# Kernel optimization log

Measured on AMD Instinct MI355X. Metric: run time of the kernel, lower is better.

The kernel has to match this reference:

```python
import jax, jax.numpy as jnp
import numpy as np

B, N, C = 2, 1024, 768
H = 12            # num_heads
HP = 24           # H_prime
HD = C // H       # head_dim = 64
KS = 3            # local conv kernel size
SCALE = HD ** -0.5


def setup_inputs() -> dict:
    key = jax.random.key(0)
    ks = jax.random.split(key, 9)
    s = lambda fan_in: 1.0 / np.sqrt(fan_in)
    return {
        "x": jax.random.normal(ks[0], (B, N, C), jnp.float32),
        "W_qk": jax.random.normal(ks[1], (2 * C, C), jnp.float32) * s(C),
        "W_v": jax.random.normal(ks[2], (C, C), jnp.float32) * s(C),
        "W_exp": jax.random.normal(ks[3], (HP, H), jnp.float32) * s(H),      # 1x1 conv H->HP
        "W_loc": jax.random.normal(ks[4], (HP, 1, KS, KS), jnp.float32) * s(KS * KS),  # depthwise 3x3
        "b_loc": jnp.zeros((HP,), jnp.float32),
        "W_red": jax.random.normal(ks[5], (H, HP), jnp.float32) * s(HP),    # 1x1 conv HP->H
        "W_proj": jax.random.normal(ks[6], (C, C), jnp.float32) * s(C),
        "b_proj": jnp.zeros((C,), jnp.float32),
    }


def _forward(x, W_qk, W_v, W_exp, W_loc, b_loc, W_red, W_proj, b_proj):
    b, n, c = x.shape
    # Attention: qk projection -> (2,B,H,N,HD)
    qk = (x @ W_qk.T).reshape(b, n, 2, H, HD).transpose(2, 0, 3, 1, 4)
    q, k = qk[0], qk[1]                                   # (B,H,N,HD)
    v = (x @ W_v.T).reshape(b, n, H, HD).transpose(0, 2, 1, 3)  # (B,H,N,HD)
    attn = jax.nn.softmax(jnp.einsum('bhnd,bhmd->bhnm', q, k) * SCALE, axis=-1)  # (B,H,N,N)

    # TokenSelector: conv-based reweighting of the attention map
    A_exp = jnp.einsum('oi,binm->bonm', W_exp, attn)      # 1x1 expand -> (B,HP,N,N)
    A_loc = jax.lax.conv_general_dilated(
        A_exp, W_loc, window_strides=(1, 1), padding='SAME',
        dimension_numbers=('NCHW', 'OIHW', 'NCHW'),
        feature_group_count=HP) + b_loc[None, :, None, None]
    A_loc = jax.nn.relu(A_loc)
    A_red = jnp.einsum('oi,binm->bonm', W_red, A_loc) * SCALE  # (B,H,N,N)
    attn2 = jax.nn.softmax(A_red, axis=-1)

    out = jnp.einsum('bhnm,bhmd->bhnd', attn2, v)         # (B,H,N,HD)
    out = out.transpose(0, 2, 1, 3).reshape(b, n, c)      # (B,N,C)
    out = out @ W_proj.T + b_proj
    return out, A_exp


def reference(x, W_qk, W_v, W_exp, W_loc, b_loc, W_red, W_proj, b_proj):
    return _forward(x, W_qk, W_v, W_exp, W_loc, b_loc, W_red, W_proj, b_proj)
```

## Files before the change

kernel.cpp:

```cpp
#include <hip/hip_runtime.h>
#include <math.h>

#define BB    2
#define NN    1024
#define CC    768
#define HH    12
#define HPP   24
#define HD    64
#define SCALE 0.125f

typedef float fvec4 __attribute__((ext_vector_type(4)));

#define SEG   (2*1024*768)
#define QOFF  0
#define KOFF  (SEG)
#define VOFF  (2*SEG)
#define HOFF  (3*SEG)

#define ASTR 132
#define BSTR 68

__global__ __launch_bounds__(256)
void qkv_gemm(const float* __restrict__ x, const float* __restrict__ Wqk,
              const float* __restrict__ Wv, float* __restrict__ ws)
{
    __shared__ float As[2][16*ASTR];
    __shared__ float Bs[2][16*BSTR];
    float* qtok = ws + QOFF;
    float* kt   = ws + KOFF;
    float* vws  = ws + VOFF;

    const int tid = threadIdx.x;
    const int bn  = blockIdx.x;
    const int bm  = blockIdx.y;
    const int tx  = tid & 15, ty = tid >> 4;

    const int am  = tid >> 1, ak = (tid & 1) * 8;
    const int bnr = tid >> 2, bk = (tid & 3) * 4;

    const float* Ap = x + (size_t)(bm*128 + am) * 768 + ak;
    const int jrow  = bn*64 + bnr;
    const float* Bp = (jrow < 1536) ? (Wqk + (size_t)jrow * 768 + bk)
                                    : (Wv  + (size_t)(jrow - 1536) * 768 + bk);

    float acc[8][4] = {};

    float4 a0 = *(const float4*)(Ap);
    float4 a1 = *(const float4*)(Ap + 4);
    float4 bv = *(const float4*)(Bp);
#pragma unroll
    for (int j = 0; j < 4; ++j) {
        As[0][(ak+j)*ASTR + am]   = ((const float*)&a0)[j];
        As[0][(ak+4+j)*ASTR + am] = ((const float*)&a1)[j];
        Bs[0][(bk+j)*BSTR + bnr]  = ((const float*)&bv)[j];
    }
    __syncthreads();

    for (int t = 0; t < 48; ++t) {
        const int cur = t & 1;
        if (t < 47) {
            a0 = *(const float4*)(Ap + (t+1)*16);
            a1 = *(const float4*)(Ap + (t+1)*16 + 4);
            bv = *(const float4*)(Bp + (t+1)*16);
        }
        const float* Asb = As[cur];
        const float* Bsb = Bs[cur];
#pragma unroll
        for (int kk = 0; kk < 16; ++kk) {
            float a[8], b[4];
#pragma unroll
            for (int i = 0; i < 8; ++i) a[i] = Asb[kk*ASTR + ty*8 + i];
#pragma unroll
            for (int j = 0; j < 4; ++j) b[j] = Bsb[kk*BSTR + tx*4 + j];
#pragma unroll
            for (int i = 0; i < 8; ++i)
#pragma unroll
                for (int j = 0; j < 4; ++j)
                    acc[i][j] = fmaf(a[i], b[j], acc[i][j]);
        }
        if (t < 47) {
#pragma unroll
            for (int j = 0; j < 4; ++j) {
                As[cur^1][(ak+j)*ASTR + am]   = ((const float*)&a0)[j];
                As[cur^1][(ak+4+j)*ASTR + am] = ((const float*)&a1)[j];
                Bs[cur^1][(bk+j)*BSTR + bnr]  = ((const float*)&bv)[j];
            }
        }
        __syncthreads();
    }

    const int colbase = bn*64 + tx*4;
    if (colbase < 768) {
#pragma unroll
        for (int i = 0; i < 8; ++i) {
            const int trow = bm*128 + ty*8 + i;
            float4 o = {acc[i][0], acc[i][1], acc[i][2], acc[i][3]};
            *(float4*)(qtok + (size_t)trow*768 + colbase) = o;
        }
    } else if (colbase < 1536) {
        const int p = colbase - 768;
#pragma unroll
        for (int i = 0; i < 8; ++i) {
            const int trow = bm*128 + ty*8 + i;
            const int b = trow >> 10, n = trow & 1023;
#pragma unroll
            for (int j = 0; j < 4; ++j)
                kt[((size_t)(b*768 + p + j))*NN + n] = acc[i][j];
        }
    } else {
        const int p = colbase - 1536;
#pragma unroll
        for (int i = 0; i < 8; ++i) {
            const int trow = bm*128 + ty*8 + i;
            const int b = trow >> 10, n = trow & 1023;
            float4 o = {acc[i][0], acc[i][1], acc[i][2], acc[i][3]};
            *(float4*)(vws + (((size_t)b*HH + (p >> 6))*NN + n)*HD + (p & 63)) = o;
        }
    }
}

__global__ __launch_bounds__(256, 2)
void attn_expand(const float* __restrict__ qtok, const float* __restrict__ kt,
                 const float* __restrict__ Wexp, float* __restrict__ aexp)
{
    __shared__ __align__(16) float qs[2*CC];
    __shared__ float wexp_s[HPP * HH];
    __shared__ float smax[2][HH * 4];
    __shared__ float ssum[2][HH * 4];

    const int tid  = threadIdx.x;
    const int lane = tid & 63, wid = tid >> 6;
    const int x    = blockIdx.x & 7;
    const int b    = x >> 2;
    const int np   = ((x & 3) << 7) | (blockIdx.x >> 3);
    const int n0   = np << 1;
    const int m4   = tid;

    const fvec4* qsrc = (const fvec4*)(qtok + (size_t)(b*NN + n0) * CC);
    ((fvec4*)qs)[tid] = qsrc[tid];
    if (tid < 128) ((fvec4*)qs)[256 + tid] = qsrc[256 + tid];
    for (int i2 = tid; i2 < HPP*HH; i2 += 256) wexp_s[i2] = Wexp[i2];
    __syncthreads();

    fvec4 l0[HH], l1[HH];
#pragma unroll
    for (int h = 0; h < HH; ++h) {
        fvec4 a0 = {0.f,0.f,0.f,0.f}, a1 = {0.f,0.f,0.f,0.f};
        const fvec4* kr = ((const fvec4*)kt) + (size_t)(b*768 + h*64) * 256 + m4;
        const float* q0p = qs + h*64;
        const float* q1p = qs + CC + h*64;
#pragma unroll 8
        for (int d = 0; d < 64; ++d) {
            const fvec4 kv = kr[(size_t)d * 256];
            const float qa = q0p[d];
            const float qb = q1p[d];
            a0.x = fmaf(kv.x, qa, a0.x); a0.y = fmaf(kv.y, qa, a0.y);
            a0.z = fmaf(kv.z, qa, a0.z); a0.w = fmaf(kv.w, qa, a0.w);
            a1.x = fmaf(kv.x, qb, a1.x); a1.y = fmaf(kv.y, qb, a1.y);
            a1.z = fmaf(kv.z, qb, a1.z); a1.w = fmaf(kv.w, qb, a1.w);
        }
        l0[h].x = a0.x*SCALE; l0[h].y = a0.y*SCALE;
        l0[h].z = a0.z*SCALE; l0[h].w = a0.w*SCALE;
        l1[h].x = a1.x*SCALE; l1[h].y = a1.y*SCALE;
        l1[h].z = a1.z*SCALE; l1[h].w = a1.w*SCALE;
    }

#pragma unroll
    for (int h = 0; h < HH; ++h) {
        float t0 = fmaxf(fmaxf(l0[h].x, l0[h].y), fmaxf(l0[h].z, l0[h].w));
        float t1 = fmaxf(fmaxf(l1[h].x, l1[h].y), fmaxf(l1[h].z, l1[h].w));
#pragma unroll
        for (int off = 32; off > 0; off >>= 1) {
            t0 = fmaxf(t0, __shfl_xor(t0, off, 64));
            t1 = fmaxf(t1, __shfl_xor(t1, off, 64));
        }
        if (lane == 0) { smax[0][h*4 + wid] = t0; smax[1][h*4 + wid] = t1; }
    }
    __syncthreads();

#pragma unroll
    for (int h = 0; h < HH; ++h) {
        const float m0 = fmaxf(fmaxf(smax[0][h*4+0], smax[0][h*4+1]),
                               fmaxf(smax[0][h*4+2], smax[0][h*4+3]));
        const float m1 = fmaxf(fmaxf(smax[1][h*4+0], smax[1][h*4+1]),
                               fmaxf(smax[1][h*4+2], smax[1][h*4+3]));
        l0[h].x = __expf(l0[h].x - m0); l0[h].y = __expf(l0[h].y - m0);
        l0[h].z = __expf(l0[h].z - m0); l0[h].w = __expf(l0[h].w - m0);
        l1[h].x = __expf(l1[h].x - m1); l1[h].y = __expf(l1[h].y - m1);
        l1[h].z = __expf(l1[h].z - m1); l1[h].w = __expf(l1[h].w - m1);
        float s0 = (l0[h].x + l0[h].y) + (l0[h].z + l0[h].w);
        float s1 = (l1[h].x + l1[h].y) + (l1[h].z + l1[h].w);
#pragma unroll
        for (int off = 32; off > 0; off >>= 1) {
            s0 += __shfl_xor(s0, off, 64);
            s1 += __shfl_xor(s1, off, 64);
        }
        if (lane == 0) { ssum[0][h*4 + wid] = s0; ssum[1][h*4 + wid] = s1; }
    }
    __syncthreads();

#pragma unroll
    for (int h = 0; h < HH; ++h) {
        const float i0 = 1.f / (ssum[0][h*4+0] + ssum[0][h*4+1] +
                                ssum[0][h*4+2] + ssum[0][h*4+3]);
        const float i1 = 1.f / (ssum[1][h*4+0] + ssum[1][h*4+1] +
                                ssum[1][h*4+2] + ssum[1][h*4+3]);
        l0[h].x *= i0; l0[h].y *= i0; l0[h].z *= i0; l0[h].w *= i0;
        l1[h].x *= i1; l1[h].y *= i1; l1[h].z *= i1; l1[h].w *= i1;
    }

    fvec4* ab = ((fvec4*)aexp) + ((size_t)b*HPP*NN + n0) * 256;
#pragma unroll 4
    for (int o = 0; o < HPP; ++o) {
        fvec4 e0 = {0.f,0.f,0.f,0.f}, e1 = {0.f,0.f,0.f,0.f};
#pragma unroll
        for (int h = 0; h < HH; ++h) {
            const float w = wexp_s[o*HH + h];
            e0.x = fmaf(w, l0[h].x, e0.x); e0.y = fmaf(w, l0[h].y, e0.y);
            e0.z = fmaf(w, l0[h].z, e0.z); e0.w = fmaf(w, l0[h].w, e0.w);
            e1.x = fmaf(w, l1[h].x, e1.x); e1.y = fmaf(w, l1[h].y, e1.y);
            e1.z = fmaf(w, l1[h].z, e1.z); e1.w = fmaf(w, l1[h].w, e1.w);
        }
        fvec4* p0 = ab + (size_t)o * NN * 256 + m4;
        __builtin_nontemporal_store(e0, p0);
        __builtin_nontemporal_store(e1, p0 + 256);
    }
}

__global__ __launch_bounds__(512, 2)
void conv_red_pv(const float* __restrict__ aexp, const float* __restrict__ Wloc,
                 const float* __restrict__ bloc, const float* __restrict__ Wred,
                 const float* __restrict__ vws, float* __restrict__ hout)
{
    __shared__ __align__(16) float probs[8][NN];
    __shared__ float redbuf[2][HH][4];

    const int tid  = threadIdx.x;
    const int lane = tid & 63;
    const int w    = tid >> 6;
    const int tk   = w >> 2;
    const int wq   = w & 3;
    const int t    = tid & 255;

    const int x  = blockIdx.x & 7;
    const int b  = x >> 2;
    const int np = ((x & 3) << 7) | (blockIdx.x >> 3);
    const int n0 = np << 1;
    const int n  = n0 + tk;

    const bool rv0 = n > 0, rv2 = n < NN - 1;

    float4 acc[HH];
#pragma unroll
    for (int i = 0; i < HH; ++i) acc[i] = make_float4(0.f,0.f,0.f,0.f);

    auto loadch = [&](int o, float4 ld[3], float hl[3], float hr[3]) {
        const float* cb = aexp + ((size_t)(b*HPP + o) * NN + (size_t)(n-1)) * NN;
#pragma unroll
        for (int r = 0; r < 3; ++r) {
            const bool ok = (r == 0) ? rv0 : (r == 2 ? rv2 : true);
            const float* rp = cb + (size_t)r * NN;
            if (ok) {
                ld[r] = ((const float4*)rp)[t];
                hl[r] = (lane == 0  && wq > 0) ? rp[4*t - 1] : 0.f;
                hr[r] = (lane == 63 && wq < 3) ? rp[4*t + 4] : 0.f;
            } else {
                ld[r] = make_float4(0.f,0.f,0.f,0.f);
                hl[r] = 0.f; hr[r] = 0.f;
            }
        }
    };

    float4 ld[3]; float hl[3], hr[3];
    loadch(0, ld, hl, hr);

    for (int o = 0; o < HPP; ++o) {
        float4 l2[3]; float h2l[3], h2r[3];
        if (o < HPP-1) loadch(o+1, l2, h2l, h2r);

        const float* wl = Wloc + o*9;
        const float  bb = bloc[o];
        float v0 = bb, v1 = bb, v2 = bb, v3 = bb;
#pragma unroll
        for (int r = 0; r < 3; ++r) {
            const float w0 = wl[r*3+0], w1 = wl[r*3+1], w2 = wl[r*3+2];
            const float4 c = ld[r];
            float lf = __shfl_up(c.w, 1, 64);
            float rt = __shfl_down(c.x, 1, 64);
            if (lane == 0)  lf = hl[r];
            if (lane == 63) rt = hr[r];
            v0 = fmaf(w0, lf,  v0); v0 = fmaf(w1, c.x, v0); v0 = fmaf(w2, c.y, v0);
            v1 = fmaf(w0, c.x, v1); v1 = fmaf(w1, c.y, v1); v1 = fmaf(w2, c.z, v1);
            v2 = fmaf(w0, c.y, v2); v2 = fmaf(w1, c.z, v2); v2 = fmaf(w2, c.w, v2);
            v3 = fmaf(w0, c.z, v3); v3 = fmaf(w1, c.w, v3); v3 = fmaf(w2, rt,  v3);
        }
        v0 = fmaxf(v0, 0.f); v1 = fmaxf(v1, 0.f);
        v2 = fmaxf(v2, 0.f); v3 = fmaxf(v3, 0.f);
#pragma unroll
        for (int i = 0; i < HH; ++i) {
            const float wr = Wred[i*HPP + o];
            acc[i].x = fmaf(wr, v0, acc[i].x);
            acc[i].y = fmaf(wr, v1, acc[i].y);
            acc[i].z = fmaf(wr, v2, acc[i].z);
            acc[i].w = fmaf(wr, v3, acc[i].w);
        }
        if (o < HPP-1) {
#pragma unroll
            for (int r = 0; r < 3; ++r) { ld[r]=l2[r]; hl[r]=h2l[r]; hr[r]=h2r[r]; }
        }
    }
#pragma unroll
    for (int i = 0; i < HH; ++i) {
        acc[i].x *= SCALE; acc[i].y *= SCALE;
        acc[i].z *= SCALE; acc[i].w *= SCALE;
    }

#pragma unroll
    for (int i = 0; i < HH; ++i) {
        float tm = fmaxf(fmaxf(acc[i].x, acc[i].y), fmaxf(acc[i].z, acc[i].w));
#pragma unroll
        for (int off = 32; off > 0; off >>= 1) tm = fmaxf(tm, __shfl_xor(tm, off, 64));
        if (lane == 0) redbuf[tk][i][wq] = tm;
    }
    __syncthreads();
    float mh[HH];
#pragma unroll
    for (int i = 0; i < HH; ++i)
        mh[i] = fmaxf(fmaxf(redbuf[tk][i][0], redbuf[tk][i][1]),
                      fmaxf(redbuf[tk][i][2], redbuf[tk][i][3]));
    __syncthreads();

#pragma unroll
    for (int i = 0; i < HH; ++i) {
        acc[i].x = __expf(acc[i].x - mh[i]);
        acc[i].y = __expf(acc[i].y - mh[i]);
        acc[i].z = __expf(acc[i].z - mh[i]);
        acc[i].w = __expf(acc[i].w - mh[i]);
        float s = (acc[i].x + acc[i].y) + (acc[i].z + acc[i].w);
#pragma unroll
        for (int off = 32; off > 0; off >>= 1) s += __shfl_xor(s, off, 64);
        if (lane == 0) redbuf[tk][i][wq] = s;
    }
    __syncthreads();
#pragma unroll
    for (int i = 0; i < HH; ++i) {
        const float inv = 1.f / (redbuf[tk][i][0] + redbuf[tk][i][1] +
                                 redbuf[tk][i][2] + redbuf[tk][i][3]);
        acc[i].x *= inv; acc[i].y *= inv; acc[i].z *= inv; acc[i].w *= inv;
    }

    const int hq = w >> 1;
    const int dh = w & 1;
    const int mg = lane >> 3;
    const int dq = lane & 7;

    for (int g = 0; g < 3; ++g) {
        __syncthreads();
#pragma unroll
        for (int q2 = 0; q2 < 4; ++q2)
            ((float4*)&probs[q2*2 + tk][0])[t] = acc[4*g + q2];
        __syncthreads();

        const int h = 4*g + hq;
        const float4* vp = ((const float4*)vws)
                         + ((size_t)(b*HH + h) * NN) * 16 + dh*8 + dq;
        const float* p0 = &probs[hq*2 + 0][0] + mg;
        const float* p1 = &probs[hq*2 + 1][0] + mg;
        float4 a0 = make_float4(0.f,0.f,0.f,0.f);
        float4 a1 = make_float4(0.f,0.f,0.f,0.f);
#pragma unroll 8
        for (int m0 = 0; m0 < NN; m0 += 8) {
            const float  pa = p0[m0];
            const float  pb = p1[m0];
            const float4 vv = vp[(size_t)(m0 + mg) * 16];
            a0.x = fmaf(pa, vv.x, a0.x); a0.y = fmaf(pa, vv.y, a0.y);
            a0.z = fmaf(pa, vv.z, a0.z); a0.w = fmaf(pa, vv.w, a0.w);
            a1.x = fmaf(pb, vv.x, a1.x); a1.y = fmaf(pb, vv.y, a1.y);
            a1.z = fmaf(pb, vv.z, a1.z); a1.w = fmaf(pb, vv.w, a1.w);
        }
#pragma unroll
        for (int off = 8; off < 64; off <<= 1) {
            a0.x += __shfl_xor(a0.x, off, 64); a0.y += __shfl_xor(a0.y, off, 64);
            a0.z += __shfl_xor(a0.z, off, 64); a0.w += __shfl_xor(a0.w, off, 64);
            a1.x += __shfl_xor(a1.x, off, 64); a1.y += __shfl_xor(a1.y, off, 64);
            a1.z += __shfl_xor(a1.z, off, 64); a1.w += __shfl_xor(a1.w, off, 64);
        }
        if (mg == 0) {
            ((float4*)(hout + ((size_t)(b*NN + n0    ) * CC) + h*HD))[dh*8 + dq] = a0;
            ((float4*)(hout + ((size_t)(b*NN + n0 + 1) * CC) + h*HD))[dh*8 + dq] = a1;
        }
    }
}

__global__ __launch_bounds__(256)
void proj_gemm(const float* __restrict__ A, const float* __restrict__ Wp,
               const float* __restrict__ bias, float* __restrict__ out)
{
    __shared__ float As[2][16*ASTR];
    __shared__ float Bs[2][16*BSTR];

    const int tid = threadIdx.x;
    const int bn  = blockIdx.x;
    const int bm  = blockIdx.y;
    const int tx  = tid & 15, ty = tid >> 4;

    const int am  = tid >> 1, ak = (tid & 1) * 8;
    const int bnr = tid >> 2, bk = (tid & 3) * 4;

    const float* Ap = A  + (size_t)(bm*128 + am) * 768 + ak;
    const float* Bp = Wp + (size_t)(bn*64 + bnr) * 768 + bk;

    float acc[8][4] = {};

    float4 a0 = *(const float4*)(Ap);
    float4 a1 = *(const float4*)(Ap + 4);
    float4 bv = *(const float4*)(Bp);
#pragma unroll
    for (int j = 0; j < 4; ++j) {
        As[0][(ak+j)*ASTR + am]   = ((const float*)&a0)[j];
        As[0][(ak+4+j)*ASTR + am] = ((const float*)&a1)[j];
        Bs[0][(bk+j)*BSTR + bnr]  = ((const float*)&bv)[j];
    }
    __syncthreads();

    for (int t = 0; t < 48; ++t) {
        const int cur = t & 1;
        if (t < 47) {
            a0 = *(const float4*)(Ap + (t+1)*16);
            a1 = *(const float4*)(Ap + (t+1)*16 + 4);
            bv = *(const float4*)(Bp + (t+1)*16);
        }
        const float* Asb = As[cur];
        const float* Bsb = Bs[cur];
#pragma unroll
        for (int kk = 0; kk < 16; ++kk) {
            float a[8], b[4];
#pragma unroll
            for (int i = 0; i < 8; ++i) a[i] = Asb[kk*ASTR + ty*8 + i];
#pragma unroll
            for (int j = 0; j < 4; ++j) b[j] = Bsb[kk*BSTR + tx*4 + j];
#pragma unroll
            for (int i = 0; i < 8; ++i)
#pragma unroll
                for (int j = 0; j < 4; ++j)
                    acc[i][j] = fmaf(a[i], b[j], acc[i][j]);
        }
        if (t < 47) {
#pragma unroll
            for (int j = 0; j < 4; ++j) {
                As[cur^1][(ak+j)*ASTR + am]   = ((const float*)&a0)[j];
                As[cur^1][(ak+4+j)*ASTR + am] = ((const float*)&a1)[j];
                Bs[cur^1][(bk+j)*BSTR + bnr]  = ((const float*)&bv)[j];
            }
        }
        __syncthreads();
    }

    const int colbase = bn*64 + tx*4;
    const float4 bb = *(const float4*)(bias + colbase);
#pragma unroll
    for (int i = 0; i < 8; ++i) {
        const int trow = bm*128 + ty*8 + i;
        float4 o = {acc[i][0] + bb.x, acc[i][1] + bb.y,
                    acc[i][2] + bb.z, acc[i][3] + bb.w};
        *(float4*)(out + (size_t)trow*768 + colbase) = o;
    }
}

extern "C" void kernel_launch(void* const* d_in, const int* in_sizes, int n_in,
                              void* d_out, int out_size, void* d_ws, size_t ws_size,
                              hipStream_t stream)
{
    const float* x     = (const float*)d_in[0];
    const float* Wqk   = (const float*)d_in[1];
    const float* Wv    = (const float*)d_in[2];
    const float* Wexp  = (const float*)d_in[3];
    const float* Wloc  = (const float*)d_in[4];
    const float* bloc  = (const float*)d_in[5];
    const float* Wred  = (const float*)d_in[6];
    const float* Wproj = (const float*)d_in[7];
    const float* bproj = (const float*)d_in[8];

    float* out  = (float*)d_out;
    float* aexp = out + (size_t)SEG;
    float* ws   = (float*)d_ws;

    qkv_gemm   <<<dim3(36, 16), 256, 0, stream>>>(x, Wqk, Wv, ws);
    attn_expand<<<dim3(BB * NN / 2), 256, 0, stream>>>(ws + QOFF, ws + KOFF, Wexp, aexp);
    conv_red_pv<<<dim3(BB * NN / 2), 512, 0, stream>>>(aexp, Wloc, bloc, Wred,
                                                       ws + VOFF, ws + HOFF);
    proj_gemm  <<<dim3(12, 16), 256, 0, stream>>>(ws + HOFF, Wproj, bproj, out);
}
```

Before: 757.0 us.

## Process four query rows per block in conv_red_pv and vectorize GEMM LDS reads

The conv/reduce/PV kernel now uses 1024-thread blocks covering four query rows instead of two. Each V load is reused across four probability rows, and the key dimension is split in half across waves, with partial sums combined through shared memory. The conv loop is restructured into a two-channel ping-pong prefetch. Separately, both GEMMs read their shared-memory tiles as float4 vectors instead of scalars. The larger blocks raise register and LDS pressure and add an extra sync per head group.

```diff
diff --git a/kernel.cpp b/kernel.cpp
--- a/kernel.cpp
+++ b/kernel.cpp
@@ -24,8 +24,8 @@
 void qkv_gemm(const float* __restrict__ x, const float* __restrict__ Wqk,
               const float* __restrict__ Wv, float* __restrict__ ws)
 {
-    __shared__ float As[2][16*ASTR];
-    __shared__ float Bs[2][16*BSTR];
+    __shared__ __align__(16) float As[2][16*ASTR];
+    __shared__ __align__(16) float Bs[2][16*BSTR];
     float* qtok = ws + QOFF;
     float* kt   = ws + KOFF;
     float* vws  = ws + VOFF;
@@ -67,11 +67,11 @@
         const float* Bsb = Bs[cur];
 #pragma unroll
         for (int kk = 0; kk < 16; ++kk) {
-            float a[8], b[4];
-#pragma unroll
-            for (int i = 0; i < 8; ++i) a[i] = Asb[kk*ASTR + ty*8 + i];
-#pragma unroll
-            for (int j = 0; j < 4; ++j) b[j] = Bsb[kk*BSTR + tx*4 + j];
+            const float4 av0 = *(const float4*)(Asb + kk*ASTR + ty*8);
+            const float4 av1 = *(const float4*)(Asb + kk*ASTR + ty*8 + 4);
+            const float4 bvv = *(const float4*)(Bsb + kk*BSTR + tx*4);
+            const float a[8] = {av0.x,av0.y,av0.z,av0.w,av1.x,av1.y,av1.z,av1.w};
+            const float b[4] = {bvv.x,bvv.y,bvv.z,bvv.w};
 #pragma unroll
             for (int i = 0; i < 8; ++i)
 #pragma unroll
@@ -227,25 +227,26 @@
     }
 }
 
-__global__ __launch_bounds__(512, 2)
+__global__ __launch_bounds__(1024, 4)
 void conv_red_pv(const float* __restrict__ aexp, const float* __restrict__ Wloc,
                  const float* __restrict__ bloc, const float* __restrict__ Wred,
                  const float* __restrict__ vws, float* __restrict__ hout)
 {
-    __shared__ __align__(16) float probs[8][NN];
-    __shared__ float redbuf[2][HH][4];
+    __shared__ __align__(16) float probs[4][4][NN];
+    __shared__ __align__(16) float4 part[4][4][2][2][8];
+    __shared__ float redbuf[4][HH][4];
 
     const int tid  = threadIdx.x;
     const int lane = tid & 63;
     const int w    = tid >> 6;
-    const int tk   = w >> 2;
-    const int wq   = w & 3;
-    const int t    = tid & 255;
+    const int tk   = tid >> 8;
+    const int wq   = (tid >> 6) & 3;
+    const int t8   = tid & 255;
 
     const int x  = blockIdx.x & 7;
     const int b  = x >> 2;
-    const int np = ((x & 3) << 7) | (blockIdx.x >> 3);
-    const int n0 = np << 1;
+    const int np = ((x & 3) << 6) | (blockIdx.x >> 3);
+    const int n0 = np << 2;
     const int n  = n0 + tk;
 
     const bool rv0 = n > 0, rv2 = n < NN - 1;
@@ -261,9 +262,9 @@
             const bool ok = (r == 0) ? rv0 : (r == 2 ? rv2 : true);
             const float* rp = cb + (size_t)r * NN;
             if (ok) {
-                ld[r] = ((const float4*)rp)[t];
-                hl[r] = (lane == 0  && wq > 0) ? rp[4*t - 1] : 0.f;
-                hr[r] = (lane == 63 && wq < 3) ? rp[4*t + 4] : 0.f;
+                ld[r] = ((const float4*)rp)[t8];
+                hl[r] = (lane == 0  && wq > 0) ? rp[4*t8 - 1] : 0.f;
+                hr[r] = (lane == 63 && wq < 3) ? rp[4*t8 + 4] : 0.f;
             } else {
                 ld[r] = make_float4(0.f,0.f,0.f,0.f);
                 hl[r] = 0.f; hr[r] = 0.f;
@@ -271,13 +272,7 @@
         }
     };
 
-    float4 ld[3]; float hl[3], hr[3];
-    loadch(0, ld, hl, hr);
-
-    for (int o = 0; o < HPP; ++o) {
-        float4 l2[3]; float h2l[3], h2r[3];
-        if (o < HPP-1) loadch(o+1, l2, h2l, h2r);
-
+    auto convstep = [&](int o, const float4 ld[3], const float hl[3], const float hr[3]) {
         const float* wl = Wloc + o*9;
         const float  bb = bloc[o];
         float v0 = bb, v1 = bb, v2 = bb, v3 = bb;
@@ -304,10 +299,16 @@
             acc[i].z = fmaf(wr, v2, acc[i].z);
             acc[i].w = fmaf(wr, v3, acc[i].w);
         }
-        if (o < HPP-1) {
-#pragma unroll
-            for (int r = 0; r < 3; ++r) { ld[r]=l2[r]; hl[r]=h2l[r]; hr[r]=h2r[r]; }
-        }
+    };
+
+    float4 ldA[3], ldB[3]; float hlA[3], hrA[3], hlB[3], hrB[3];
+    loadch(0, ldA, hlA, hrA);
+    loadch(1, ldB, hlB, hrB);
+    for (int o = 0; o < HPP; o += 2) {
+        convstep(o, ldA, hlA, hrA);
+        if (o + 2 < HPP) loadch(o + 2, ldA, hlA, hrA);
+        convstep(o + 1, ldB, hlB, hrB);
+        if (o + 3 < HPP) loadch(o + 3, ldB, hlB, hrB);
     }
 #pragma unroll
     for (int i = 0; i < HH; ++i) {
@@ -323,19 +324,19 @@
         if (lane == 0) redbuf[tk][i][wq] = tm;
     }
     __syncthreads();
-    float mh[HH];
+    float mh_[HH];
 #pragma unroll
     for (int i = 0; i < HH; ++i)
-        mh[i] = fmaxf(fmaxf(redbuf[tk][i][0], redbuf[tk][i][1]),
-                      fmaxf(redbuf[tk][i][2], redbuf[tk][i][3]));
+        mh_[i] = fmaxf(fmaxf(redbuf[tk][i][0], redbuf[tk][i][1]),
+                       fmaxf(redbuf[tk][i][2], redbuf[tk][i][3]));
     __syncthreads();
 
 #pragma unroll
     for (int i = 0; i < HH; ++i) {
-        acc[i].x = __expf(acc[i].x - mh[i]);
-        acc[i].y = __expf(acc[i].y - mh[i]);
-        acc[i].z = __expf(acc[i].z - mh[i]);
-        acc[i].w = __expf(acc[i].w - mh[i]);
+        acc[i].x = __expf(acc[i].x - mh_[i]);
+        acc[i].y = __expf(acc[i].y - mh_[i]);
+        acc[i].z = __expf(acc[i].z - mh_[i]);
+        acc[i].w = __expf(acc[i].w - mh_[i]);
         float s = (acc[i].x + acc[i].y) + (acc[i].z + acc[i].w);
 #pragma unroll
         for (int off = 32; off > 0; off >>= 1) s += __shfl_xor(s, off, 64);
@@ -349,8 +350,9 @@
         acc[i].x *= inv; acc[i].y *= inv; acc[i].z *= inv; acc[i].w *= inv;
     }
 
-    const int hq = w >> 1;
-    const int dh = w & 1;
+    const int hq = w & 3;
+    const int dh = (w >> 2) & 1;
+    const int mhf = w >> 3;
     const int mg = lane >> 3;
     const int dq = lane & 7;
 
@@ -358,25 +360,34 @@
         __syncthreads();
 #pragma unroll
         for (int q2 = 0; q2 < 4; ++q2)
-            ((float4*)&probs[q2*2 + tk][0])[t] = acc[4*g + q2];
+            ((float4*)&probs[tk][q2][0])[t8] = acc[g*4 + q2];
         __syncthreads();
 
-        const int h = 4*g + hq;
+        const int h = g*4 + hq;
         const float4* vp = ((const float4*)vws)
                          + ((size_t)(b*HH + h) * NN) * 16 + dh*8 + dq;
-        const float* p0 = &probs[hq*2 + 0][0] + mg;
-        const float* p1 = &probs[hq*2 + 1][0] + mg;
+        const float* pr0 = &probs[0][hq][0];
+        const float* pr1 = &probs[1][hq][0];
+        const float* pr2 = &probs[2][hq][0];
+        const float* pr3 = &probs[3][hq][0];
+        const int mbase = mhf*512 + mg;
         float4 a0 = make_float4(0.f,0.f,0.f,0.f);
         float4 a1 = make_float4(0.f,0.f,0.f,0.f);
+        float4 a2 = make_float4(0.f,0.f,0.f,0.f);
+        float4 a3 = make_float4(0.f,0.f,0.f,0.f);
 #pragma unroll 8
-        for (int m0 = 0; m0 < NN; m0 += 8) {
-            const float  pa = p0[m0];
-            const float  pb = p1[m0];
-            const float4 vv = vp[(size_t)(m0 + mg) * 16];
-            a0.x = fmaf(pa, vv.x, a0.x); a0.y = fmaf(pa, vv.y, a0.y);
-            a0.z = fmaf(pa, vv.z, a0.z); a0.w = fmaf(pa, vv.w, a0.w);
-            a1.x = fmaf(pb, vv.x, a1.x); a1.y = fmaf(pb, vv.y, a1.y);
-            a1.z = fmaf(pb, vv.z, a1.z); a1.w = fmaf(pb, vv.w, a1.w);
+        for (int it = 0; it < 64; ++it) {
+            const int m = mbase + it*8;
+            const float4 vv = vp[(size_t)m * 16];
+            const float p0 = pr0[m], p1 = pr1[m], p2 = pr2[m], p3 = pr3[m];
+            a0.x = fmaf(p0, vv.x, a0.x); a0.y = fmaf(p0, vv.y, a0.y);
+            a0.z = fmaf(p0, vv.z, a0.z); a0.w = fmaf(p0, vv.w, a0.w);
+            a1.x = fmaf(p1, vv.x, a1.x); a1.y = fmaf(p1, vv.y, a1.y);
+            a1.z = fmaf(p1, vv.z, a1.z); a1.w = fmaf(p1, vv.w, a1.w);
+            a2.x = fmaf(p2, vv.x, a2.x); a2.y = fmaf(p2, vv.y, a2.y);
+            a2.z = fmaf(p2, vv.z, a2.z); a2.w = fmaf(p2, vv.w, a2.w);
+            a3.x = fmaf(p3, vv.x, a3.x); a3.y = fmaf(p3, vv.y, a3.y);
+            a3.z = fmaf(p3, vv.z, a3.z); a3.w = fmaf(p3, vv.w, a3.w);
         }
 #pragma unroll
         for (int off = 8; off < 64; off <<= 1) {
@@ -384,10 +395,26 @@
             a0.z += __shfl_xor(a0.z, off, 64); a0.w += __shfl_xor(a0.w, off, 64);
             a1.x += __shfl_xor(a1.x, off, 64); a1.y += __shfl_xor(a1.y, off, 64);
             a1.z += __shfl_xor(a1.z, off, 64); a1.w += __shfl_xor(a1.w, off, 64);
+            a2.x += __shfl_xor(a2.x, off, 64); a2.y += __shfl_xor(a2.y, off, 64);
+            a2.z += __shfl_xor(a2.z, off, 64); a2.w += __shfl_xor(a2.w, off, 64);
+            a3.x += __shfl_xor(a3.x, off, 64); a3.y += __shfl_xor(a3.y, off, 64);
+            a3.z += __shfl_xor(a3.z, off, 64); a3.w += __shfl_xor(a3.w, off, 64);
         }
         if (mg == 0) {
-            ((float4*)(hout + ((size_t)(b*NN + n0    ) * CC) + h*HD))[dh*8 + dq] = a0;
-            ((float4*)(hout + ((size_t)(b*NN + n0 + 1) * CC) + h*HD))[dh*8 + dq] = a1;
+            part[0][hq][dh][mhf][dq] = a0;
+            part[1][hq][dh][mhf][dq] = a1;
+            part[2][hq][dh][mhf][dq] = a2;
+            part[3][hq][dh][mhf][dq] = a3;
+        }
+        __syncthreads();
+        if (lane < 16) {
+            const int tok = w >> 2, hq2 = w & 3;
+            const int dh2 = lane >> 3, dq2 = lane & 7;
+            const float4 s0 = part[tok][hq2][dh2][0][dq2];
+            const float4 s1 = part[tok][hq2][dh2][1][dq2];
+            float4 sum = {s0.x+s1.x, s0.y+s1.y, s0.z+s1.z, s0.w+s1.w};
+            *(float4*)(hout + ((size_t)(b*NN + n0 + tok))*CC
+                       + (g*4+hq2)*HD + dh2*32 + dq2*4) = sum;
         }
     }
 }
@@ -396,8 +423,8 @@
 void proj_gemm(const float* __restrict__ A, const float* __restrict__ Wp,
                const float* __restrict__ bias, float* __restrict__ out)
 {
-    __shared__ float As[2][16*ASTR];
-    __shared__ float Bs[2][16*BSTR];
+    __shared__ __align__(16) float As[2][16*ASTR];
+    __shared__ __align__(16) float Bs[2][16*BSTR];
 
     const int tid = threadIdx.x;
     const int bn  = blockIdx.x;
@@ -434,11 +461,11 @@
         const float* Bsb = Bs[cur];
 #pragma unroll
         for (int kk = 0; kk < 16; ++kk) {
-            float a[8], b[4];
-#pragma unroll
-            for (int i = 0; i < 8; ++i) a[i] = Asb[kk*ASTR + ty*8 + i];
-#pragma unroll
-            for (int j = 0; j < 4; ++j) b[j] = Bsb[kk*BSTR + tx*4 + j];
+            const float4 av0 = *(const float4*)(Asb + kk*ASTR + ty*8);
+            const float4 av1 = *(const float4*)(Asb + kk*ASTR + ty*8 + 4);
+            const float4 bvv = *(const float4*)(Bsb + kk*BSTR + tx*4);
+            const float a[8] = {av0.x,av0.y,av0.z,av0.w,av1.x,av1.y,av1.z,av1.w};
+            const float b[4] = {bvv.x,bvv.y,bvv.z,bvv.w};
 #pragma unroll
             for (int i = 0; i < 8; ++i)
 #pragma unroll
@@ -487,7 +514,7 @@
 
     qkv_gemm   <<<dim3(36, 16), 256, 0, stream>>>(x, Wqk, Wv, ws);
     attn_expand<<<dim3(BB * NN / 2), 256, 0, stream>>>(ws + QOFF, ws + KOFF, Wexp, aexp);
-    conv_red_pv<<<dim3(BB * NN / 2), 512, 0, stream>>>(aexp, Wloc, bloc, Wred,
-                                                       ws + VOFF, ws + HOFF);
+    conv_red_pv<<<dim3(BB * NN / 4), 1024, 0, stream>>>(aexp, Wloc, bloc, Wred,
+                                                        ws + VOFF, ws + HOFF);
     proj_gemm  <<<dim3(12, 16), 256, 0, stream>>>(ws + HOFF, Wproj, bproj, out);
 }
```

Result: slower. 872.5 us (+15.3%).
